# Kernel tuning notes

Measured on AMD Instinct MI355X. Metric: run time of the kernel, lower is better.

Reference implementation:

```python
import jax, jax.numpy as jnp
import numpy as np

R, C = 30, 56
N = R * C  # 1680
K = 0.005
PRCN = 15
ALPHA = 1.0
BETA = 1.0


def setup_inputs() -> dict:
    key = jax.random.key(0)
    k1, k2 = jax.random.split(key)
    net_in = jax.random.normal(k1, (2 * N,), dtype=jnp.float32)
    # Recurrent connectivity matrix (learned weight in the original, loaded from .mat)
    J = jax.random.normal(k2, (N, N), dtype=jnp.float32) / np.float32(np.sqrt(N))
    return {"net_in": net_in, "J": J}


def reference(net_in, J):
    Iext = net_in[:N].reshape(R, C)
    r0 = net_in[N:2 * N].reshape(R, C)

    def step(r, _):
        # 4-way chunked mm + cat in the original == single matvec J @ r_flat
        temp = (J @ r.reshape(N)).reshape(R, C)
        U = ALPHA * (BETA * temp) + ALPHA * Iext
        sq = jnp.square(0.2 * U)
        recSum = jnp.sum(K * sq)
        # (0.2*U)^2 * (0.04 / recSum) / 0.04  ==  sq / recSum, kept explicit for fidelity
        r_new = sq * (0.04 / recSum) / 0.04
        return r_new, (U, recSum)

    r_last, (Us, sums) = jax.lax.scan(step, r0, None, length=PRCN - 1)
    return Us[-1], sums[-1], r_last
```

## Files before the change

kernel.cpp:

```cpp
#include <hip/hip_runtime.h>


#define N      1680
#define NV4    420
#define NSTEP  14
#define GBLK   105
#define RPB    16
#define RPW    4

__device__ __forceinline__ float llc_load(const float* p) {
    return __hip_atomic_load(p, __ATOMIC_RELAXED, __HIP_MEMORY_SCOPE_AGENT);
}
__device__ __forceinline__ void llc_store(float* p, float v) {
    __hip_atomic_store(p, v, __ATOMIC_RELAXED, __HIP_MEMORY_SCOPE_AGENT);
}

__global__ __launch_bounds__(256, 1) void fused_recur(
    const float* __restrict__ J,
    const float* __restrict__ net_in,
    float* __restrict__ out,
    float* __restrict__ ws)
{
    __shared__ float r_lds[N];
    __shared__ float sred[4];
    __shared__ float wsq[4];

    float* partials = ws;
    float* rbuf0    = ws + 1472;
    float* rbuf1    = ws + 1472 + 1792;

    const int tid  = threadIdx.x;
    const int lane = tid & 63;
    const int wave = tid >> 6;
    const int row0 = blockIdx.x * RPB + wave * RPW;

    float4 Jr[RPW][7];
    #pragma unroll
    for (int m = 0; m < RPW; ++m) {
        const float4* Jrow = (const float4*)(J + (size_t)(row0 + m) * N);
        #pragma unroll
        for (int k = 0; k < 7; ++k) {
            const int idx = lane + 64 * k;
            Jr[m][k] = (idx < NV4) ? Jrow[idx] : make_float4(0.f, 0.f, 0.f, 0.f);
        }
    }
    float iext[RPW];
    #pragma unroll
    for (int m = 0; m < RPW; ++m) iext[m] = net_in[row0 + m];

    float Uv[RPW], Qv[RPW];
    float4* rl4 = (float4*)r_lds;

    for (int t = 0; t < NSTEP; ++t) {
        float s_prev;
        if (t == 0) {
            const float4* rs4 = (const float4*)(net_in + N);
            for (int i = tid; i < NV4; i += 256) rl4[i] = rs4[i];
            if (lane == 0) sred[wave] = 0.0f;
            __syncthreads();
            s_prev = 1.0f;
        } else {
            const float* pp = partials + (t - 1) * GBLK;
            float v = 0.0f;
            if (tid < GBLK) {
                do { v = llc_load(pp + tid); } while (!(v >= 0.0f));
            }
            float p = v;
            #pragma unroll
            for (int off = 32; off; off >>= 1) p += __shfl_xor(p, off, 64);
            if (lane == 0) sred[wave] = p;
            __syncthreads();
            s_prev = sred[0] + sred[1] + sred[2] + sred[3];

            const float* rsrc = (t & 1) ? rbuf0 : rbuf1;
            float rv_s[7];
            #pragma unroll
            for (int k = 0; k < 7; ++k) {
                const int idx = tid + 256 * k;
                rv_s[k] = (idx < N) ? llc_load(rsrc + idx) : 0.0f;
            }
            #pragma unroll
            for (int k = 0; k < 7; ++k) {
                const int idx = tid + 256 * k;
                if (idx < N) r_lds[idx] = rv_s[k];
            }
            __syncthreads();
        }

        float4 rv[7];
        #pragma unroll
        for (int k = 0; k < 7; ++k) {
            const int idx = lane + 64 * k;
            rv[k] = (idx < NV4) ? rl4[idx] : make_float4(0.f, 0.f, 0.f, 0.f);
        }

        float a[RPW];
        #pragma unroll
        for (int m = 0; m < RPW; ++m) {
            float acc = 0.0f;
            #pragma unroll
            for (int k = 0; k < 7; ++k) {
                acc += Jr[m][k].x * rv[k].x;
                acc += Jr[m][k].y * rv[k].y;
                acc += Jr[m][k].z * rv[k].z;
                acc += Jr[m][k].w * rv[k].w;
            }
            a[m] = acc;
        }
        #pragma unroll
        for (int off = 32; off; off >>= 1) {
            #pragma unroll
            for (int m = 0; m < RPW; ++m) a[m] += __shfl_xor(a[m], off, 64);
        }

        float psum = 0.0f;
        #pragma unroll
        for (int m = 0; m < RPW; ++m) {
            const float U  = a[m] / s_prev + iext[m];
            const float u2 = 0.2f * U;
            const float sq = u2 * u2;
            Uv[m] = U;
            Qv[m] = sq;
            psum += sq;
        }

        if (lane == 0) {
            wsq[wave] = 0.005f * psum;
            if (t < NSTEP - 1) {
                float* wb = (t & 1) ? rbuf1 : rbuf0;
                llc_store(wb + row0 + 0, Qv[0]);
                llc_store(wb + row0 + 1, Qv[1]);
                llc_store(wb + row0 + 2, Qv[2]);
                llc_store(wb + row0 + 3, Qv[3]);
            }
        }
        __syncthreads();
        if (tid == 0) {
            llc_store(partials + t * GBLK + blockIdx.x,
                      wsq[0] + wsq[1] + wsq[2] + wsq[3]);
        }
    }

    {
        const float* pp = partials + (NSTEP - 1) * GBLK;
        float v = 0.0f;
        if (tid < GBLK) {
            do { v = llc_load(pp + tid); } while (!(v >= 0.0f));
        }
        float p = v;
        #pragma unroll
        for (int off = 32; off; off >>= 1) p += __shfl_xor(p, off, 64);
        if (lane == 0) sred[wave] = p;
        __syncthreads();
    }
    const float s13 = sred[0] + sred[1] + sred[2] + sred[3];

    if (lane == 0)
        *(float4*)(out + row0) = make_float4(Uv[0], Uv[1], Uv[2], Uv[3]);
    if (lane < RPW) {
        const float q = (lane == 0) ? Qv[0] : (lane == 1) ? Qv[1]
                       : (lane == 2) ? Qv[2] : Qv[3];
        out[N + 1 + row0 + lane] = q / s13;
    }
    if (blockIdx.x == 0 && tid == 0) out[N] = s13;
}

extern "C" void kernel_launch(void* const* d_in, const int* in_sizes, int n_in,
                              void* d_out, int out_size, void* d_ws, size_t ws_size,
                              hipStream_t stream) {
    const float* net_in = (const float*)d_in[0];
    const float* J      = (const float*)d_in[1];
    hipMemsetAsync(d_ws, 0xBF, NSTEP * GBLK * sizeof(float), stream);
    fused_recur<<<GBLK, 256, 0, stream>>>(J, net_in, (float*)d_out, (float*)d_ws);
}
```

Before: 130.8 us.

## Replace per-block partial sums with per-step r buffers polled via dwordx4 loads

Each block now writes its squared outputs into a step-indexed buffer that is pre-filled with a negative sentinel. Consumers poll these values directly with vectorised cache-bypassing loads and compute the normalising sum locally from the full r vector. This drops the separate partials array and the extra barrier and atomic store that published them, so each step has one cross-block dependency instead of two. The cost is a larger memset, polling on 1680 values instead of 105, and inline asm that waits on vmcnt(0) after every load.

```diff
diff --git a/kernel.cpp b/kernel.cpp
--- a/kernel.cpp
+++ b/kernel.cpp
@@ -1,5 +1,7 @@
 #include <hip/hip_runtime.h>
 
+
+typedef float f32x4 __attribute__((ext_vector_type(4)));
 
 #define N      1680
 #define NV4    420
@@ -8,11 +10,16 @@
 #define RPB    16
 #define RPW    4
 
-__device__ __forceinline__ float llc_load(const float* p) {
-    return __hip_atomic_load(p, __ATOMIC_RELAXED, __HIP_MEMORY_SCOPE_AGENT);
+__device__ __forceinline__ f32x4 llc_load4(const f32x4* p) {
+    f32x4 v;
+    asm volatile("global_load_dwordx4 %0, %1, off sc0 sc1\n\t"
+                 "s_waitcnt vmcnt(0)"
+                 : "=v"(v) : "v"(p) : "memory");
+    return v;
 }
-__device__ __forceinline__ void llc_store(float* p, float v) {
-    __hip_atomic_store(p, v, __ATOMIC_RELAXED, __HIP_MEMORY_SCOPE_AGENT);
+__device__ __forceinline__ void llc_store4(f32x4* p, f32x4 v) {
+    asm volatile("global_store_dwordx4 %0, %1, off sc0 sc1"
+                 :: "v"(p), "v"(v) : "memory");
 }
 
 __global__ __launch_bounds__(256, 1) void fused_recur(
@@ -21,89 +28,92 @@
     float* __restrict__ out,
     float* __restrict__ ws)
 {
-    __shared__ float r_lds[N];
+    __shared__ f32x4 r_lds[NV4];
     __shared__ float sred[4];
-    __shared__ float wsq[4];
 
-    float* partials = ws;
-    float* rbuf0    = ws + 1472;
-    float* rbuf1    = ws + 1472 + 1792;
+    f32x4* bufs = (f32x4*)ws;
 
     const int tid  = threadIdx.x;
     const int lane = tid & 63;
     const int wave = tid >> 6;
-    const int row0 = blockIdx.x * RPB + wave * RPW;
+    const int row0 = (int)blockIdx.x * RPB + wave * RPW;
 
-    float4 Jr[RPW][7];
+    f32x4 Jr[RPW][7];
     #pragma unroll
     for (int m = 0; m < RPW; ++m) {
-        const float4* Jrow = (const float4*)(J + (size_t)(row0 + m) * N);
+        const f32x4* Jrow = (const f32x4*)(J + (size_t)(row0 + m) * N);
         #pragma unroll
         for (int k = 0; k < 7; ++k) {
             const int idx = lane + 64 * k;
-            Jr[m][k] = (idx < NV4) ? Jrow[idx] : make_float4(0.f, 0.f, 0.f, 0.f);
+            Jr[m][k] = (idx < NV4) ? Jrow[idx] : (f32x4)0.f;
         }
     }
+    #pragma unroll
+    for (int m = 0; m < RPW; ++m)
+        #pragma unroll
+        for (int k = 0; k < 7; ++k)
+            asm volatile("" : "+v"(Jr[m][k]));
+
     float iext[RPW];
     #pragma unroll
     for (int m = 0; m < RPW; ++m) iext[m] = net_in[row0 + m];
 
     float Uv[RPW], Qv[RPW];
-    float4* rl4 = (float4*)r_lds;
 
+    {
+        const f32x4* r0 = (const f32x4*)(net_in + N);
+        for (int i = tid; i < NV4; i += 256) r_lds[i] = r0[i];
+    }
+    __syncthreads();
+    float s_prev = 1.0f;
+
+    #pragma unroll 1
     for (int t = 0; t < NSTEP; ++t) {
-        float s_prev;
-        if (t == 0) {
-            const float4* rs4 = (const float4*)(net_in + N);
-            for (int i = tid; i < NV4; i += 256) rl4[i] = rs4[i];
-            if (lane == 0) sred[wave] = 0.0f;
-            __syncthreads();
-            s_prev = 1.0f;
-        } else {
-            const float* pp = partials + (t - 1) * GBLK;
-            float v = 0.0f;
-            if (tid < GBLK) {
-                do { v = llc_load(pp + tid); } while (!(v >= 0.0f));
+        if (t > 0) {
+            f32x4* src = bufs + (size_t)(t - 1) * NV4;
+            f32x4 v0 = (f32x4)0.f, v1 = (f32x4)0.f;
+            float psum;
+            {
+                const f32x4* p0 = src + tid;
+                do { v0 = llc_load4(p0); }
+                while (!(v0[0] >= 0.f && v0[1] >= 0.f &&
+                         v0[2] >= 0.f && v0[3] >= 0.f));
+                psum = (v0[0] + v0[1]) + (v0[2] + v0[3]);
             }
-            float p = v;
-            #pragma unroll
-            for (int off = 32; off; off >>= 1) p += __shfl_xor(p, off, 64);
-            if (lane == 0) sred[wave] = p;
-            __syncthreads();
-            s_prev = sred[0] + sred[1] + sred[2] + sred[3];
-
-            const float* rsrc = (t & 1) ? rbuf0 : rbuf1;
-            float rv_s[7];
-            #pragma unroll
-            for (int k = 0; k < 7; ++k) {
-                const int idx = tid + 256 * k;
-                rv_s[k] = (idx < N) ? llc_load(rsrc + idx) : 0.0f;
+            const int i1 = tid + 256;
+            if (i1 < NV4) {
+                const f32x4* p1 = src + i1;
+                do { v1 = llc_load4(p1); }
+                while (!(v1[0] >= 0.f && v1[1] >= 0.f &&
+                         v1[2] >= 0.f && v1[3] >= 0.f));
+                psum += (v1[0] + v1[1]) + (v1[2] + v1[3]);
             }
             #pragma unroll
-            for (int k = 0; k < 7; ++k) {
-                const int idx = tid + 256 * k;
-                if (idx < N) r_lds[idx] = rv_s[k];
-            }
+            for (int off = 32; off; off >>= 1) psum += __shfl_xor(psum, off, 64);
+            if (lane == 0) sred[wave] = psum;
+            r_lds[tid] = v0;
+            if (i1 < NV4) r_lds[i1] = v1;
             __syncthreads();
+            s_prev = 0.005f * ((sred[0] + sred[1]) + (sred[2] + sred[3]));
         }
 
-        float4 rv[7];
+        f32x4 rv[7];
         #pragma unroll
         for (int k = 0; k < 7; ++k) {
             const int idx = lane + 64 * k;
-            rv[k] = (idx < NV4) ? rl4[idx] : make_float4(0.f, 0.f, 0.f, 0.f);
+            rv[k] = (idx < NV4) ? r_lds[idx] : (f32x4)0.f;
         }
 
         float a[RPW];
         #pragma unroll
         for (int m = 0; m < RPW; ++m) {
-            float acc = 0.0f;
+            float acc = 0.f;
             #pragma unroll
             for (int k = 0; k < 7; ++k) {
-                acc += Jr[m][k].x * rv[k].x;
-                acc += Jr[m][k].y * rv[k].y;
-                acc += Jr[m][k].z * rv[k].z;
-                acc += Jr[m][k].w * rv[k].w;
+                acc += Jr[m][k][0] * rv[k][0];
+                acc += Jr[m][k][1] * rv[k][1];
+                acc += Jr[m][k][2] * rv[k][2];
+                acc += Jr[m][k][3] * rv[k][3];
             }
             a[m] = acc;
         }
@@ -113,50 +123,52 @@
             for (int m = 0; m < RPW; ++m) a[m] += __shfl_xor(a[m], off, 64);
         }
 
-        float psum = 0.0f;
         #pragma unroll
         for (int m = 0; m < RPW; ++m) {
             const float U  = a[m] / s_prev + iext[m];
             const float u2 = 0.2f * U;
-            const float sq = u2 * u2;
             Uv[m] = U;
-            Qv[m] = sq;
-            psum += sq;
+            Qv[m] = u2 * u2;
         }
 
         if (lane == 0) {
-            wsq[wave] = 0.005f * psum;
-            if (t < NSTEP - 1) {
-                float* wb = (t & 1) ? rbuf1 : rbuf0;
-                llc_store(wb + row0 + 0, Qv[0]);
-                llc_store(wb + row0 + 1, Qv[1]);
-                llc_store(wb + row0 + 2, Qv[2]);
-                llc_store(wb + row0 + 3, Qv[3]);
-            }
+            f32x4 q4 = { Qv[0], Qv[1], Qv[2], Qv[3] };
+            llc_store4(bufs + (size_t)t * NV4 + (row0 >> 2), q4);
         }
         __syncthreads();
-        if (tid == 0) {
-            llc_store(partials + t * GBLK + blockIdx.x,
-                      wsq[0] + wsq[1] + wsq[2] + wsq[3]);
-        }
     }
 
     {
-        const float* pp = partials + (NSTEP - 1) * GBLK;
-        float v = 0.0f;
-        if (tid < GBLK) {
-            do { v = llc_load(pp + tid); } while (!(v >= 0.0f));
+        f32x4* src = bufs + (size_t)(NSTEP - 1) * NV4;
+        f32x4 v0;
+        float psum;
+        {
+            const f32x4* p0 = src + tid;
+            do { v0 = llc_load4(p0); }
+            while (!(v0[0] >= 0.f && v0[1] >= 0.f &&
+                     v0[2] >= 0.f && v0[3] >= 0.f));
+            psum = (v0[0] + v0[1]) + (v0[2] + v0[3]);
         }
-        float p = v;
+        const int i1 = tid + 256;
+        if (i1 < NV4) {
+            const f32x4* p1 = src + i1;
+            f32x4 v1;
+            do { v1 = llc_load4(p1); }
+            while (!(v1[0] >= 0.f && v1[1] >= 0.f &&
+                     v1[2] >= 0.f && v1[3] >= 0.f));
+            psum += (v1[0] + v1[1]) + (v1[2] + v1[3]);
+        }
         #pragma unroll
-        for (int off = 32; off; off >>= 1) p += __shfl_xor(p, off, 64);
-        if (lane == 0) sred[wave] = p;
+        for (int off = 32; off; off >>= 1) psum += __shfl_xor(psum, off, 64);
+        if (lane == 0) sred[wave] = psum;
         __syncthreads();
     }
-    const float s13 = sred[0] + sred[1] + sred[2] + sred[3];
+    const float s13 = 0.005f * ((sred[0] + sred[1]) + (sred[2] + sred[3]));
 
-    if (lane == 0)
-        *(float4*)(out + row0) = make_float4(Uv[0], Uv[1], Uv[2], Uv[3]);
+    if (lane == 0) {
+        f32x4 u4 = { Uv[0], Uv[1], Uv[2], Uv[3] };
+        *(f32x4*)(out + row0) = u4;
+    }
     if (lane < RPW) {
         const float q = (lane == 0) ? Qv[0] : (lane == 1) ? Qv[1]
                        : (lane == 2) ? Qv[2] : Qv[3];
@@ -170,6 +182,6 @@
                               hipStream_t stream) {
     const float* net_in = (const float*)d_in[0];
     const float* J      = (const float*)d_in[1];
-    hipMemsetAsync(d_ws, 0xBF, NSTEP * GBLK * sizeof(float), stream);
+    hipMemsetAsync(d_ws, 0xBF, (size_t)NSTEP * NV4 * sizeof(f32x4), stream);
     fused_recur<<<GBLK, 256, 0, stream>>>(J, net_in, (float*)d_out, (float*)d_ws);
 }
```

Result: faster. 109.3 us (-16.4%).
